# Kernel tuning notes

Hardware: AMD Instinct MI355X
Metric: run time of the kernel (lower is better)

## Reference

```python
import jax, jax.numpy as jnp
import numpy as np

B, T, L, E, H, V = 128, 16, 196, 512, 1024, 32000


def setup_inputs() -> dict:
    key = jax.random.key(0)
    ks = jax.random.split(key, 20)
    s = 0.02
    return {
        "caption_in": jax.random.randint(ks[0], (B, T), 0, V),
        "image_feats": jax.random.normal(ks[1], (B, L, E), jnp.float32),
        "emb": jax.random.normal(ks[2], (V, E), jnp.float32) * s,
        "W_init_h": jax.random.normal(ks[3], (E, H), jnp.float32) * s,
        "b_init_h": jnp.zeros((H,), jnp.float32),
        "W_init_c": jax.random.normal(ks[4], (E, H), jnp.float32) * s,
        "b_init_c": jnp.zeros((H,), jnp.float32),
        "W_a": jax.random.normal(ks[5], (H, H), jnp.float32) * s,
        "b_a": jnp.zeros((H,), jnp.float32),
        "U_a": jax.random.normal(ks[6], (E, H), jnp.float32) * s,
        "b_ua": jnp.zeros((H,), jnp.float32),
        "V_a": jax.random.normal(ks[7], (H, 1), jnp.float32) * s,
        "b_va": jnp.zeros((1,), jnp.float32),
        "W_beta": jax.random.normal(ks[8], (H, E), jnp.float32) * s,
        "b_beta": jnp.zeros((E,), jnp.float32),
        "W_lstm": jax.random.normal(ks[9], (2 * E, 4 * H), jnp.float32) * s,
        "U_lstm": jax.random.normal(ks[10], (H, 4 * H), jnp.float32) * s,
        "b_lstm": jnp.zeros((4 * H,), jnp.float32),
        "W_out": jax.random.normal(ks[11], (H, V), jnp.float32) * s,
        "b_out": jnp.zeros((V,), jnp.float32),
    }


def _decode(caption_in, image_feats, emb, W_init_h, b_init_h, W_init_c, b_init_c,
            W_a, b_a, U_a, b_ua, V_a, b_va, W_beta, b_beta,
            W_lstm, U_lstm, b_lstm, W_out, b_out):
    cap_emb = emb[caption_in]                      # [B,T,E]
    mean_a = jnp.mean(image_feats, axis=1)         # [B,E]
    h0 = mean_a @ W_init_h + b_init_h              # [B,H]
    c0 = mean_a @ W_init_c + b_init_c
    # attention keys: precompute U_a(h_list) once (same math as in-loop)
    keys = jnp.einsum('ble,eh->blh', image_feats, U_a) + b_ua  # [B,L,H]

    def step(carry, x_t):                          # x_t: [B,E]
        h, c = carry
        q = h @ W_a + b_a                          # [B,H]
        e = jax.nn.relu(q[:, None, :] + keys) @ V_a + b_va  # [B,L,1]
        alpha = jax.nn.softmax(e, axis=1)          # [B,L,1]
        z = jnp.sum(alpha * image_feats, axis=1)   # [B,E]
        z = z * jax.nn.sigmoid(h @ W_beta + b_beta)
        ctx = jnp.concatenate([z, x_t], axis=-1)   # [B,2E]
        gates = ctx @ W_lstm + h @ U_lstm + b_lstm # [B,4H]
        i, f, g, o = jnp.split(gates, 4, axis=-1)  # keras order i,f,c,o
        c_new = jax.nn.sigmoid(f) * c + jax.nn.sigmoid(i) * jnp.tanh(g)
        h_new = jax.nn.sigmoid(o) * jnp.tanh(c_new)
        out = jax.nn.softmax(h_new @ W_out + b_out, axis=-1)  # [B,V]
        return (h_new, c_new), out

    xs = jnp.transpose(cap_emb, (1, 0, 2))         # [T,B,E]
    _, outs = jax.lax.scan(step, (h0, c0), xs)     # [T,B,V]
    return jnp.transpose(outs, (1, 0, 2))          # [B,T,V]


def reference(caption_in, image_feats, emb, W_init_h, b_init_h, W_init_c, b_init_c,
              W_a, b_a, U_a, b_ua, V_a, b_va, W_beta, b_beta,
              W_lstm, U_lstm, b_lstm, W_out, b_out):
    return _decode(caption_in, image_feats, emb, W_init_h, b_init_h, W_init_c, b_init_c,
                   W_a, b_a, U_a, b_ua, V_a, b_va, W_beta, b_beta,
                   W_lstm, U_lstm, b_lstm, W_out, b_out)
```

## Files before the change

kernel.cpp:

```cpp
#include <hip/hip_runtime.h>
#include <hip/hip_bf16.h>
#include <math.h>

constexpr int Bc = 128, Tc = 16, Lc = 196, Ec = 512, Hc = 1024, Vc = 32000;

typedef float f32x4_t __attribute__((ext_vector_type(4)));
typedef short s16x8_t __attribute__((ext_vector_type(8)));

__device__ __forceinline__ float sigmoidf_(float x) { return 1.0f / (1.0f + expf(-x)); }

__device__ __forceinline__ unsigned short bf16rn(float x) {
    union { float f; unsigned u; } v; v.f = x;
    unsigned r = v.u + 0x7fffu + ((v.u >> 16) & 1u);
    return (unsigned short)(r >> 16);
}
__device__ __forceinline__ float bf16tof(unsigned short h) {
    union { unsigned u; float f; } v; v.u = ((unsigned)h) << 16; return v.f;
}

__global__ __launch_bounds__(256)
void transpose_split(const float* __restrict__ src, int N,
                     unsigned short* __restrict__ dhi, unsigned short* __restrict__ dlo,
                     int ldd)
{
    __shared__ float tile[32][33];
    const int k0 = blockIdx.x * 32, n0 = blockIdx.y * 32;
    const int tx = threadIdx.x & 31, ty = threadIdx.x >> 5;
#pragma unroll
    for (int i = 0; i < 4; ++i)
        tile[ty + i * 8][tx] = src[(size_t)(k0 + ty + i * 8) * N + n0 + tx];
    __syncthreads();
#pragma unroll
    for (int i = 0; i < 4; ++i) {
        int nl = ty + i * 8;
        float v = tile[tx][nl];
        unsigned short hi = bf16rn(v);
        unsigned short lo = bf16rn(v - bf16tof(hi));
        size_t off = (size_t)(n0 + nl) * ldd + k0 + tx;
        dhi[off] = hi;
        dlo[off] = lo;
    }
}

__global__ __launch_bounds__(256)
void gemm_mfma_split(const float* __restrict__ A, int lda,
                     const unsigned short* __restrict__ Bhi,
                     const unsigned short* __restrict__ Blo,
                     float* __restrict__ C, long ldc,
                     const float* __restrict__ bias, int K, long cslice)
{
    __shared__ __align__(16) unsigned short As_hi[2][128][32];
    __shared__ __align__(16) unsigned short As_lo[2][128][32];
    __shared__ __align__(16) unsigned short Bs_hi[2][128][32];
    __shared__ __align__(16) unsigned short Bs_lo[2][128][32];

    const int t = threadIdx.x;
    const int wave = t >> 6, lane = t & 63;
    const int wr = wave >> 1, wc = wave & 1;
    const int lm = lane & 15, qd = lane >> 4;
    const size_t m0 = (size_t)blockIdx.x * 128;
    const size_t n0 = (size_t)blockIdx.y * 128;

    const int S   = gridDim.z;
    const int ksl = blockIdx.z;
    const int Ksl = K / S;
    const int kbase = ksl * Ksl;

    const int srow = t >> 1;
    const int skh  = (t & 1) * 16;

    const float* Ap = A + (m0 + srow) * (size_t)lda + skh + kbase;
    const unsigned short* Bhp = Bhi + (n0 + srow) * (size_t)K + skh + kbase;
    const unsigned short* Blp = Blo + (n0 + srow) * (size_t)K + skh + kbase;

    const int nk = Ksl >> 5;
    float* Cp = C + (size_t)ksl * cslice;

    f32x4_t acc[4][4];
#pragma unroll
    for (int i = 0; i < 4; ++i)
#pragma unroll
        for (int j = 0; j < 4; ++j)
            acc[i][j] = (f32x4_t){0.f, 0.f, 0.f, 0.f};

    float av[16];
    s16x8_t sbh0, sbh1, sbl0, sbl1;

#define G_LOAD(k0_)                                              \
    do {                                                         \
        *(float4*)&av[0]  = *(const float4*)(Ap + (k0_));        \
        *(float4*)&av[4]  = *(const float4*)(Ap + (k0_) + 4);    \
        *(float4*)&av[8]  = *(const float4*)(Ap + (k0_) + 8);    \
        *(float4*)&av[12] = *(const float4*)(Ap + (k0_) + 12);   \
        sbh0 = *(const s16x8_t*)(Bhp + (k0_));                   \
        sbh1 = *(const s16x8_t*)(Bhp + (k0_) + 8);               \
        sbl0 = *(const s16x8_t*)(Blp + (k0_));                   \
        sbl1 = *(const s16x8_t*)(Blp + (k0_) + 8);               \
    } while (0)

#define LDS_STORE(buf_)                                          \
    do {                                                         \
        s16x8_t h0, h1, l0, l1;                                  \
        _Pragma("unroll")                                        \
        for (int i = 0; i < 8; ++i) {                            \
            unsigned short hi = bf16rn(av[i]);                   \
            h0[i] = (short)hi;                                   \
            l0[i] = (short)bf16rn(av[i] - bf16tof(hi));          \
        }                                                        \
        _Pragma("unroll")                                        \
        for (int i = 0; i < 8; ++i) {                            \
            unsigned short hi = bf16rn(av[8 + i]);               \
            h1[i] = (short)hi;                                   \
            l1[i] = (short)bf16rn(av[8 + i] - bf16tof(hi));      \
        }                                                        \
        *(s16x8_t*)&As_hi[buf_][srow][skh]     = h0;             \
        *(s16x8_t*)&As_hi[buf_][srow][skh + 8] = h1;             \
        *(s16x8_t*)&As_lo[buf_][srow][skh]     = l0;             \
        *(s16x8_t*)&As_lo[buf_][srow][skh + 8] = l1;             \
        *(s16x8_t*)&Bs_hi[buf_][srow][skh]     = sbh0;           \
        *(s16x8_t*)&Bs_hi[buf_][srow][skh + 8] = sbh1;           \
        *(s16x8_t*)&Bs_lo[buf_][srow][skh]     = sbl0;           \
        *(s16x8_t*)&Bs_lo[buf_][srow][skh + 8] = sbl1;           \
    } while (0)

    G_LOAD(0);
    LDS_STORE(0);
    if (nk > 1) G_LOAD(32);
    __syncthreads();

    for (int k = 0; k < nk; ++k) {
        const int cur = k & 1;
        s16x8_t ah[4], al[4], bh[4], bl[4];
#pragma unroll
        for (int mt = 0; mt < 4; ++mt) {
            ah[mt] = *(const s16x8_t*)&As_hi[cur][wr * 64 + mt * 16 + lm][qd * 8];
            al[mt] = *(const s16x8_t*)&As_lo[cur][wr * 64 + mt * 16 + lm][qd * 8];
        }
#pragma unroll
        for (int nt = 0; nt < 4; ++nt) {
            bh[nt] = *(const s16x8_t*)&Bs_hi[cur][wc * 64 + nt * 16 + lm][qd * 8];
            bl[nt] = *(const s16x8_t*)&Bs_lo[cur][wc * 64 + nt * 16 + lm][qd * 8];
        }
        if (k + 1 < nk) {
            LDS_STORE(cur ^ 1);
            if (k + 2 < nk) G_LOAD((k + 2) << 5);
        }
#pragma unroll
        for (int mt = 0; mt < 4; ++mt)
#pragma unroll
            for (int nt = 0; nt < 4; ++nt) {
                acc[mt][nt] = __builtin_amdgcn_mfma_f32_16x16x32_bf16(ah[mt], bh[nt], acc[mt][nt], 0, 0, 0);
                acc[mt][nt] = __builtin_amdgcn_mfma_f32_16x16x32_bf16(ah[mt], bl[nt], acc[mt][nt], 0, 0, 0);
                acc[mt][nt] = __builtin_amdgcn_mfma_f32_16x16x32_bf16(al[mt], bh[nt], acc[mt][nt], 0, 0, 0);
            }
        __syncthreads();
    }
#undef G_LOAD
#undef LDS_STORE

#pragma unroll
    for (int nt = 0; nt < 4; ++nt) {
        size_t n = n0 + wc * 64 + nt * 16 + lm;
        float bs = bias ? bias[n] : 0.f;
#pragma unroll
        for (int mt = 0; mt < 4; ++mt) {
#pragma unroll
            for (int r = 0; r < 4; ++r) {
                size_t m = m0 + wr * 64 + mt * 16 + qd * 4 + r;
                Cp[(size_t)m * ldc + n] = acc[mt][nt][r] + bs;
            }
        }
    }
}

__global__ __launch_bounds__(256)
void concat2(const float* __restrict__ a, int na, const float* __restrict__ b, int nb,
             float* __restrict__ out)
{
    int i = blockIdx.x * 256 + threadIdx.x;
    if (i < na) out[i] = a[i];
    else if (i < na + nb) out[i] = b[i - na];
}

__global__ __launch_bounds__(256)
void mean_kernel(const float* __restrict__ feats, float* __restrict__ mean_a)
{
    int b = blockIdx.x;
    int e = blockIdx.y * 256 + threadIdx.x;
    const float* f = feats + ((size_t)b * Lc) * Ec + e;
    float s = 0.f;
    for (int l = 0; l < Lc; ++l) s += f[(size_t)l * Ec];
    mean_a[b * Ec + e] = s * (1.0f / Lc);
}

__global__ __launch_bounds__(256)
void att_scores_sk(const float* __restrict__ qp, long qstride,
                   const float* __restrict__ b_a,
                   const float* __restrict__ keys,
                   const float* __restrict__ V_a, const float* __restrict__ b_va,
                   float* __restrict__ e)
{
    int pair = blockIdx.x * 4 + (threadIdx.x >> 6);
    int lane = threadIdx.x & 63;
    int b = pair / Lc;
    const float* kp = keys + (size_t)pair * Hc;
    const float* q0 = qp + (size_t)b * 1536;
    float s = 0.f;
    for (int h = lane; h < Hc; h += 64) {
        float q = b_a[h] + q0[h] + q0[qstride + h] + q0[2 * qstride + h] + q0[3 * qstride + h];
        s = fmaf(fmaxf(q + kp[h], 0.f), V_a[h], s);
    }
#pragma unroll
    for (int off = 32; off > 0; off >>= 1) s += __shfl_down(s, off);
    if (lane == 0) e[pair] = s + b_va[0];
}

__global__ __launch_bounds__(256)
void zxcat_fused(const float* __restrict__ e,
                 const float* __restrict__ qp, long qstride,
                 const float* __restrict__ b_beta,
                 const int* __restrict__ caption, const float* __restrict__ emb,
                 const float* __restrict__ feats, const float* __restrict__ hc,
                 float* __restrict__ xcat, int t)
{
    int b = blockIdx.x;
    int j = blockIdx.y * 256 + threadIdx.x;
    if (blockIdx.y < 2) {
        __shared__ float red[256];
        __shared__ float alpha[Lc];
        int tid = threadIdx.x;
        float ev = (tid < Lc) ? e[b * Lc + tid] : -1e30f;
        red[tid] = ev; __syncthreads();
        for (int s = 128; s > 0; s >>= 1) { if (tid < s) red[tid] = fmaxf(red[tid], red[tid + s]); __syncthreads(); }
        float m = red[0]; __syncthreads();
        float ex = (tid < Lc) ? expf(ev - m) : 0.f;
        red[tid] = ex; __syncthreads();
        for (int s = 128; s > 0; s >>= 1) { if (tid < s) red[tid] += red[tid + s]; __syncthreads(); }
        float ssum = red[0];
        if (tid < Lc) alpha[tid] = ex / ssum;
        __syncthreads();
        const float* f = feats + ((size_t)b * Lc) * Ec + j;
        float s = 0.f;
        for (int l = 0; l < Lc; ++l) s = fmaf(alpha[l], f[(size_t)l * Ec], s);
        const float* q0 = qp + (size_t)b * 1536 + 1024 + j;
        float sb = b_beta[j] + q0[0] + q0[qstride] + q0[2 * qstride] + q0[3 * qstride];
        xcat[(size_t)b * 2048 + j] = s * sigmoidf_(sb);
    } else if (j < 2 * Ec) {
        int tok = caption[b * Tc + t];
        xcat[(size_t)b * 2048 + j] = emb[(size_t)tok * Ec + (j - Ec)];
    } else {
        xcat[(size_t)b * 2048 + j] = hc[(size_t)b * 2048 + (j - 2 * Ec)];
    }
}

__global__ __launch_bounds__(256)
void lstm_elem_sk(const float* __restrict__ gp, long gstride,
                  const float* __restrict__ b_lstm,
                  float* __restrict__ hbase, float* __restrict__ cbase, int ld)
{
    int idx = blockIdx.x * 256 + threadIdx.x;
    int b = idx >> 10;
    int j = idx & (Hc - 1);
    float gi = b_lstm[j], gf = b_lstm[Hc + j], gg = b_lstm[2 * Hc + j], go = b_lstm[3 * Hc + j];
#pragma unroll
    for (int s = 0; s < 4; ++s) {
        const float* g = gp + (size_t)s * gstride + (size_t)b * 4 * Hc;
        gi += g[j]; gf += g[Hc + j]; gg += g[2 * Hc + j]; go += g[3 * Hc + j];
    }
    float* cp = cbase + (size_t)b * ld + j;
    float* hp = hbase + (size_t)b * ld + j;
    float cn = sigmoidf_(gf) * (*cp) + sigmoidf_(gi) * tanhf(gg);
    *cp = cn;
    *hp = sigmoidf_(go) * tanhf(cn);
}

__global__ __launch_bounds__(1024)
void softmax_V(float* __restrict__ out, int t)
{
    int b = blockIdx.x;
    float* p = out + ((size_t)b * Tc + t) * (size_t)Vc;
    __shared__ float red[1024];
    int tid = threadIdx.x;
    float m = -1e30f;
    for (int v = tid; v < Vc; v += 1024) m = fmaxf(m, p[v]);
    red[tid] = m; __syncthreads();
    for (int s = 512; s > 0; s >>= 1) { if (tid < s) red[tid] = fmaxf(red[tid], red[tid + s]); __syncthreads(); }
    m = red[0]; __syncthreads();
    float sum = 0.f;
    for (int v = tid; v < Vc; v += 1024) sum += expf(p[v] - m);
    red[tid] = sum; __syncthreads();
    for (int s = 512; s > 0; s >>= 1) { if (tid < s) red[tid] += red[tid + s]; __syncthreads(); }
    float inv = 1.0f / red[0];
    for (int v = tid; v < Vc; v += 1024) p[v] = expf(p[v] - m) * inv;
}

__global__ __launch_bounds__(256)
void att_scores(const float* __restrict__ q, int ldq, const float* __restrict__ keys,
                const float* __restrict__ V_a, const float* __restrict__ b_va,
                float* __restrict__ e)
{
    int pair = blockIdx.x * 4 + (threadIdx.x >> 6);
    int lane = threadIdx.x & 63;
    int b = pair / Lc;
    const float* qp = q + (size_t)b * ldq;
    const float* kp = keys + (size_t)pair * Hc;
    float s = 0.f;
    for (int h = lane; h < Hc; h += 64)
        s = fmaf(fmaxf(qp[h] + kp[h], 0.f), V_a[h], s);
#pragma unroll
    for (int off = 32; off > 0; off >>= 1) s += __shfl_down(s, off);
    if (lane == 0) e[pair] = s + b_va[0];
}

__global__ __launch_bounds__(256)
void softmax_L(float* __restrict__ e)
{
    int b = blockIdx.x;
    float* p = e + b * Lc;
    __shared__ float red[256];
    int tid = threadIdx.x;
    float m = -1e30f;
    if (tid < Lc) m = p[tid];
    red[tid] = m; __syncthreads();
    for (int s = 128; s > 0; s >>= 1) { if (tid < s) red[tid] = fmaxf(red[tid], red[tid + s]); __syncthreads(); }
    m = red[0]; __syncthreads();
    float ex = 0.f;
    if (tid < Lc) ex = expf(p[tid] - m);
    red[tid] = ex; __syncthreads();
    for (int s = 128; s > 0; s >>= 1) { if (tid < s) red[tid] += red[tid + s]; __syncthreads(); }
    if (tid < Lc) p[tid] = ex / red[0];
}

__global__ __launch_bounds__(256)
void z_kernel(const float* __restrict__ alpha, const float* __restrict__ feats,
              float* __restrict__ z)
{
    int b = blockIdx.x;
    int e = blockIdx.y * 256 + threadIdx.x;
    const float* f = feats + ((size_t)b * Lc) * Ec + e;
    const float* a = alpha + b * Lc;
    float s = 0.f;
    for (int l = 0; l < Lc; ++l) s = fmaf(a[l], f[(size_t)l * Ec], s);
    z[b * Ec + e] = s;
}

__global__ __launch_bounds__(256)
void ctx_build(const float* __restrict__ z, const float* __restrict__ sb,
               const int* __restrict__ caption, const float* __restrict__ emb,
               float* __restrict__ ctx, int t)
{
    int b = blockIdx.x;
    int j = blockIdx.y * 256 + threadIdx.x;
    float v;
    if (j < Ec) {
        v = z[b * Ec + j] * sigmoidf_(sb[b * Ec + j]);
    } else {
        int tok = caption[b * Tc + t];
        v = emb[(size_t)tok * Ec + (j - Ec)];
    }
    ctx[b * (2 * Ec) + j] = v;
}

__global__ __launch_bounds__(256)
void lstm_elem(const float* __restrict__ gates, float* __restrict__ hbase,
               float* __restrict__ cbase, int ld)
{
    int idx = blockIdx.x * 256 + threadIdx.x;
    int b = idx >> 10;
    int j = idx & (Hc - 1);
    const float* g = gates + (size_t)b * 4 * Hc;
    float gi = g[j], gf = g[Hc + j], gg = g[2 * Hc + j], go = g[3 * Hc + j];
    float* cp = cbase + (size_t)b * ld + j;
    float* hp = hbase + (size_t)b * ld + j;
    float cn = sigmoidf_(gf) * (*cp) + sigmoidf_(gi) * tanhf(gg);
    *cp = cn;
    *hp = sigmoidf_(go) * tanhf(cn);
}

__global__ __launch_bounds__(256)
void gemm_f32(const float* __restrict__ A, int lda,
              const float* __restrict__ Bm, int ldb,
              float* __restrict__ C, int ldc,
              const float* __restrict__ bias,
              int K, int accumulate)
{
    __shared__ __align__(16) float As[16][68];
    __shared__ __align__(16) float Bs[16][68];
    const int t  = threadIdx.x;
    const int tx = t & 15;
    const int ty = t >> 4;
    const size_t m0 = (size_t)blockIdx.x * 64;
    const size_t n0 = (size_t)blockIdx.y * 64;
    const int arow = t >> 2;
    const int acol = (t & 3) << 2;
    const int brow = t >> 4;
    const int bcol = (t & 15) << 2;
    const float* Aptr = A + (m0 + arow) * (size_t)lda + acol;
    const float* Bptr = Bm + (size_t)brow * ldb + n0 + bcol;
    float acc[4][4] = {};
    for (int k0 = 0; k0 < K; k0 += 16) {
        float4 av = *reinterpret_cast<const float4*>(Aptr + k0);
        float4 bv = *reinterpret_cast<const float4*>(Bptr + (size_t)k0 * ldb);
        As[acol + 0][arow] = av.x;
        As[acol + 1][arow] = av.y;
        As[acol + 2][arow] = av.z;
        As[acol + 3][arow] = av.w;
        *reinterpret_cast<float4*>(&Bs[brow][bcol]) = bv;
        __syncthreads();
#pragma unroll
        for (int k = 0; k < 16; ++k) {
            float4 a4 = *reinterpret_cast<const float4*>(&As[k][ty << 2]);
            float4 b4 = *reinterpret_cast<const float4*>(&Bs[k][tx << 2]);
            float aa[4] = {a4.x, a4.y, a4.z, a4.w};
            float bb[4] = {b4.x, b4.y, b4.z, b4.w};
#pragma unroll
            for (int i = 0; i < 4; ++i)
#pragma unroll
                for (int j = 0; j < 4; ++j)
                    acc[i][j] = fmaf(aa[i], bb[j], acc[i][j]);
        }
        __syncthreads();
    }
    float4 bv4 = {0.f, 0.f, 0.f, 0.f};
    if (bias) bv4 = *reinterpret_cast<const float4*>(&bias[n0 + (tx << 2)]);
#pragma unroll
    for (int i = 0; i < 4; ++i) {
        size_t off = (m0 + (size_t)(ty << 2) + i) * (size_t)ldc + n0 + (tx << 2);
        float4 o;
        o.x = acc[i][0] + bv4.x;
        o.y = acc[i][1] + bv4.y;
        o.z = acc[i][2] + bv4.z;
        o.w = acc[i][3] + bv4.w;
        if (accumulate) {
            float4 prev = *reinterpret_cast<const float4*>(&C[off]);
            o.x += prev.x; o.y += prev.y; o.z += prev.z; o.w += prev.w;
        }
        *reinterpret_cast<float4*>(&C[off]) = o;
    }
}

extern "C" void kernel_launch(void* const* d_in, const int* in_sizes, int n_in,
                              void* d_out, int out_size, void* d_ws, size_t ws_size,
                              hipStream_t stream)
{
    const int*   caption  = (const int*)  d_in[0];
    const float* feats    = (const float*)d_in[1];
    const float* emb      = (const float*)d_in[2];
    const float* W_init_h = (const float*)d_in[3];
    const float* b_init_h = (const float*)d_in[4];
    const float* W_init_c = (const float*)d_in[5];
    const float* b_init_c = (const float*)d_in[6];
    const float* W_a      = (const float*)d_in[7];
    const float* b_a      = (const float*)d_in[8];
    const float* U_a      = (const float*)d_in[9];
    const float* b_ua     = (const float*)d_in[10];
    const float* V_a      = (const float*)d_in[11];
    const float* b_va     = (const float*)d_in[12];
    const float* W_beta   = (const float*)d_in[13];
    const float* b_beta   = (const float*)d_in[14];
    const float* W_lstm   = (const float*)d_in[15];
    const float* U_lstm   = (const float*)d_in[16];
    const float* b_lstm   = (const float*)d_in[17];
    const float* W_out    = (const float*)d_in[18];
    const float* b_out    = (const float*)d_in[19];
    float* out = (float*)d_out;

    dim3 blk(256);

    char* base = (char*)d_ws;
    size_t off = 0;
    auto alloc = [&](size_t bytes) { char* p = base + off; off = (off + bytes + 15) & ~(size_t)15; return p; };

    float* keys      = (float*)alloc((size_t)Bc * Lc * Hc * 4);
    float* hc        = (float*)alloc((size_t)Bc * 2048 * 4);
    float* qsb_part  = (float*)alloc((size_t)4 * Bc * 1536 * 4);
    float* e         = (float*)alloc((size_t)Bc * Lc * 4);
    float* xcat      = (float*)alloc((size_t)Bc * 2048 * 4);
    float* gate_part = (float*)alloc((size_t)4 * Bc * 4 * Hc * 4);
    float* mean_a    = (float*)alloc((size_t)Bc * Ec * 4);
    float* bcat_i    = (float*)alloc(2048 * 4);
    unsigned short* Wout_hi  = (unsigned short*)alloc((size_t)Vc * Hc * 2);
    unsigned short* Wout_lo  = (unsigned short*)alloc((size_t)Vc * Hc * 2);
    unsigned short* Wg_hi    = (unsigned short*)alloc((size_t)4096 * 2048 * 2);
    unsigned short* Wg_lo    = (unsigned short*)alloc((size_t)4096 * 2048 * 2);
    unsigned short* Wqsb_hi  = (unsigned short*)alloc((size_t)1536 * 1024 * 2);
    unsigned short* Wqsb_lo  = (unsigned short*)alloc((size_t)1536 * 1024 * 2);
    unsigned short* Ua_hi    = (unsigned short*)alloc((size_t)1024 * 512 * 2);
    unsigned short* Ua_lo    = (unsigned short*)alloc((size_t)1024 * 512 * 2);
    unsigned short* Wini_hi  = (unsigned short*)alloc((size_t)2048 * 512 * 2);
    unsigned short* Wini_lo  = (unsigned short*)alloc((size_t)2048 * 512 * 2);
    const size_t need_fast = off;

    const long QSTRIDE = (long)Bc * 1536;
    const long GSTRIDE = (long)Bc * 4 * Hc;

    if (ws_size >= need_fast) {
        transpose_split<<<dim3(16, 32), blk, 0, stream>>>(U_a, 1024, Ua_hi, Ua_lo, 512);
        transpose_split<<<dim3(16, 32), blk, 0, stream>>>(W_init_h, 1024, Wini_hi, Wini_lo, 512);
        transpose_split<<<dim3(16, 32), blk, 0, stream>>>(W_init_c, 1024, Wini_hi + (size_t)1024 * 512, Wini_lo + (size_t)1024 * 512, 512);
        transpose_split<<<dim3(32, 32), blk, 0, stream>>>(W_a, 1024, Wqsb_hi, Wqsb_lo, 1024);
        transpose_split<<<dim3(32, 16), blk, 0, stream>>>(W_beta, 512, Wqsb_hi + (size_t)1024 * 1024, Wqsb_lo + (size_t)1024 * 1024, 1024);
        transpose_split<<<dim3(32, 128), blk, 0, stream>>>(W_lstm, 4096, Wg_hi, Wg_lo, 2048);
        transpose_split<<<dim3(32, 128), blk, 0, stream>>>(U_lstm, 4096, Wg_hi + 1024, Wg_lo + 1024, 2048);
        transpose_split<<<dim3(32, 1000), blk, 0, stream>>>(W_out, Vc, Wout_hi, Wout_lo, 1024);
        concat2<<<dim3(8), blk, 0, stream>>>(b_init_h, 1024, b_init_c, 1024, bcat_i);

        mean_kernel<<<dim3(Bc, 2), blk, 0, stream>>>(feats, mean_a);
        gemm_mfma_split<<<dim3(1, 16, 1), blk, 0, stream>>>(mean_a, Ec, Wini_hi, Wini_lo, hc, 2048, bcat_i, 512, 0);
        gemm_mfma_split<<<dim3((Bc * Lc) / 128, 8, 1), blk, 0, stream>>>(feats, Ec, Ua_hi, Ua_lo, keys, Hc, b_ua, 512, 0);

        for (int t = 0; t < Tc; ++t) {
            gemm_mfma_split<<<dim3(1, 12, 4), blk, 0, stream>>>(hc, 2048, Wqsb_hi, Wqsb_lo, qsb_part, 1536, nullptr, 1024, QSTRIDE);
            att_scores_sk<<<dim3((Bc * Lc) / 4), blk, 0, stream>>>(qsb_part, QSTRIDE, b_a, keys, V_a, b_va, e);
            zxcat_fused<<<dim3(Bc, 8), blk, 0, stream>>>(e, qsb_part, QSTRIDE, b_beta, caption, emb, feats, hc, xcat, t);
            gemm_mfma_split<<<dim3(1, 32, 4), blk, 0, stream>>>(xcat, 2048, Wg_hi, Wg_lo, gate_part, 4096, nullptr, 2048, GSTRIDE);
            lstm_elem_sk<<<dim3((Bc * Hc) / 256), blk, 0, stream>>>(gate_part, GSTRIDE, b_lstm, hc, hc + 1024, 2048);
            gemm_mfma_split<<<dim3(1, 250, 1), blk, 0, stream>>>(hc, 2048, Wout_hi, Wout_lo, out + (size_t)t * Vc, (long)Tc * Vc, b_out, 1024, 0);
            softmax_V<<<dim3(Bc), dim3(1024), 0, stream>>>(out, t);
        }
        return;
    }

    float* ws = (float*)d_ws;
    size_t foff = 0;
    float* l_keys  = ws + foff; foff += (size_t)Bc * Lc * Hc;
    float* l_h     = ws + foff; foff += (size_t)Bc * Hc;
    float* l_c     = ws + foff; foff += (size_t)Bc * Hc;
    float* l_q     = ws + foff; foff += (size_t)Bc * Hc;
    float* l_e     = ws + foff; foff += (size_t)Bc * Lc;
    float* l_sb    = ws + foff; foff += (size_t)Bc * Ec;
    float* l_z     = ws + foff; foff += (size_t)Bc * Ec;
    float* l_ctx   = ws + foff; foff += (size_t)Bc * 2 * Ec;
    float* l_gates = ws + foff; foff += (size_t)Bc * 4 * Hc;
    float* l_mean  = ws + foff; foff += (size_t)Bc * Ec;
    if (ws_size < foff * sizeof(float)) return;

    mean_kernel<<<dim3(Bc, 2), blk, 0, stream>>>(feats, l_mean);
    gemm_f32<<<dim3(Bc / 64, Hc / 64), blk, 0, stream>>>(l_mean, Ec, W_init_h, Hc, l_h, Hc, b_init_h, Ec, 0);
    gemm_f32<<<dim3(Bc / 64, Hc / 64), blk, 0, stream>>>(l_mean, Ec, W_init_c, Hc, l_c, Hc, b_init_c, Ec, 0);
    gemm_f32<<<dim3((Bc * Lc) / 64, Hc / 64), blk, 0, stream>>>(feats, Ec, U_a, Hc, l_keys, Hc, b_ua, Ec, 0);
    for (int t = 0; t < Tc; ++t) {
        gemm_f32<<<dim3(Bc / 64, Hc / 64), blk, 0, stream>>>(l_h, Hc, W_a, Hc, l_q, Hc, b_a, Hc, 0);
        att_scores<<<dim3((Bc * Lc) / 4), blk, 0, stream>>>(l_q, Hc, l_keys, V_a, b_va, l_e);
        softmax_L<<<dim3(Bc), blk, 0, stream>>>(l_e);
        z_kernel<<<dim3(Bc, 2), blk, 0, stream>>>(l_e, feats, l_z);
        gemm_f32<<<dim3(Bc / 64, Ec / 64), blk, 0, stream>>>(l_h, Hc, W_beta, Ec, l_sb, Ec, b_beta, Hc, 0);
        ctx_build<<<dim3(Bc, 4), blk, 0, stream>>>(l_z, l_sb, caption, emb, l_ctx, t);
        gemm_f32<<<dim3(Bc / 64, (4 * Hc) / 64), blk, 0, stream>>>(l_ctx, 2 * Ec, W_lstm, 4 * Hc, l_gates, 4 * Hc, b_lstm, 2 * Ec, 0);
        gemm_f32<<<dim3(Bc / 64, (4 * Hc) / 64), blk, 0, stream>>>(l_h, Hc, U_lstm, 4 * Hc, l_gates, 4 * Hc, nullptr, Hc, 1);
        lstm_elem<<<dim3((Bc * Hc) / 256), blk, 0, stream>>>(l_gates, l_h, l_c, Hc);
        gemm_f32<<<dim3(Bc / 64, Vc / 64), blk, 0, stream>>>(l_h, Hc, W_out, Vc, out + (size_t)t * Vc, Tc * Vc, b_out, Hc, 0);
        softmax_V<<<dim3(Bc), dim3(1024), 0, stream>>>(out, t);
    }
}
```

Baseline: 3.286 ms.

## Merge prep transposes and fuse per-step GEMMs and softmax with attention

All weight transpose/split launches and the mean kernel are merged into one multi-descriptor prep kernel. The next step's q/beta GEMM now runs in the same launch as the vocab projection GEMM, and the vocab softmax shares a launch with the next step's attention scoring. This shifts the schedule so independent work for step t+1 overlaps step t, cutting launch count and filling idle CUs. The cost is a software pipeline that is more complex, plus blocks of mixed size inside one launch.

```diff
diff --git a/kernel.cpp b/kernel.cpp
--- a/kernel.cpp
+++ b/kernel.cpp
@@ -18,17 +18,46 @@
     union { unsigned u; float f; } v; v.u = ((unsigned)h) << 16; return v.f;
 }
 
-__global__ __launch_bounds__(256)
-void transpose_split(const float* __restrict__ src, int N,
-                     unsigned short* __restrict__ dhi, unsigned short* __restrict__ dlo,
-                     int ldd)
-{
+struct TDesc {
+    const float* src;
+    unsigned short* dhi;
+    unsigned short* dlo;
+    int N, ldd, gx, base;
+};
+struct PrepP {
+    TDesc d[8];
+    int tblocks;
+    const float* feats;
+    float* mean_a;
+};
+
+__global__ __launch_bounds__(256)
+void prep_multi(PrepP p)
+{
+    const int id = blockIdx.x;
+    if (id >= p.tblocks) {
+        int idm = id - p.tblocks;
+        int b = idm >> 1;
+        int e = (idm & 1) * 256 + threadIdx.x;
+        const float* f = p.feats + ((size_t)b * Lc) * Ec + e;
+        float s = 0.f;
+        for (int l = 0; l < Lc; ++l) s += f[(size_t)l * Ec];
+        p.mean_a[b * Ec + e] = s * (1.0f / Lc);
+        return;
+    }
+    int di = 0;
+#pragma unroll
+    for (int i = 1; i < 8; ++i) if (id >= p.d[i].base) di = i;
+    const TDesc d = p.d[di];
+    const int lid = id - d.base;
+    const int k0 = (lid % d.gx) * 32;
+    const int n0 = (lid / d.gx) * 32;
+
     __shared__ float tile[32][33];
-    const int k0 = blockIdx.x * 32, n0 = blockIdx.y * 32;
     const int tx = threadIdx.x & 31, ty = threadIdx.x >> 5;
 #pragma unroll
     for (int i = 0; i < 4; ++i)
-        tile[ty + i * 8][tx] = src[(size_t)(k0 + ty + i * 8) * N + n0 + tx];
+        tile[ty + i * 8][tx] = d.src[(size_t)(k0 + ty + i * 8) * d.N + n0 + tx];
     __syncthreads();
 #pragma unroll
     for (int i = 0; i < 4; ++i) {
@@ -36,45 +65,48 @@
         float v = tile[tx][nl];
         unsigned short hi = bf16rn(v);
         unsigned short lo = bf16rn(v - bf16tof(hi));
-        size_t off = (size_t)(n0 + nl) * ldd + k0 + tx;
-        dhi[off] = hi;
-        dlo[off] = lo;
-    }
-}
-
-__global__ __launch_bounds__(256)
-void gemm_mfma_split(const float* __restrict__ A, int lda,
-                     const unsigned short* __restrict__ Bhi,
-                     const unsigned short* __restrict__ Blo,
-                     float* __restrict__ C, long ldc,
-                     const float* __restrict__ bias, int K, long cslice)
-{
-    __shared__ __align__(16) unsigned short As_hi[2][128][32];
-    __shared__ __align__(16) unsigned short As_lo[2][128][32];
-    __shared__ __align__(16) unsigned short Bs_hi[2][128][32];
-    __shared__ __align__(16) unsigned short Bs_lo[2][128][32];
+        size_t off = (size_t)(n0 + nl) * d.ldd + k0 + tx;
+        d.dhi[off] = hi;
+        d.dlo[off] = lo;
+    }
+}
+
+struct GemmP {
+    const float* A;
+    const unsigned short* Bhi;
+    const unsigned short* Blo;
+    float* C;
+    const float* bias;
+    long ldc, cslice;
+    int lda, K, gx, gy, S;
+};
+
+__device__ __forceinline__ void gemm_body(char* smem, int bx, int by, int ksl, const GemmP& p)
+{
+    auto As_hi = (unsigned short (*)[128][32])(smem);
+    auto As_lo = (unsigned short (*)[128][32])(smem + 16384);
+    auto Bs_hi = (unsigned short (*)[128][32])(smem + 32768);
+    auto Bs_lo = (unsigned short (*)[128][32])(smem + 49152);
 
     const int t = threadIdx.x;
     const int wave = t >> 6, lane = t & 63;
     const int wr = wave >> 1, wc = wave & 1;
     const int lm = lane & 15, qd = lane >> 4;
-    const size_t m0 = (size_t)blockIdx.x * 128;
-    const size_t n0 = (size_t)blockIdx.y * 128;
-
-    const int S   = gridDim.z;
-    const int ksl = blockIdx.z;
-    const int Ksl = K / S;
+    const size_t m0 = (size_t)bx * 128;
+    const size_t n0 = (size_t)by * 128;
+
+    const int Ksl = p.K / p.S;
     const int kbase = ksl * Ksl;
 
     const int srow = t >> 1;
     const int skh  = (t & 1) * 16;
 
-    const float* Ap = A + (m0 + srow) * (size_t)lda + skh + kbase;
-    const unsigned short* Bhp = Bhi + (n0 + srow) * (size_t)K + skh + kbase;
-    const unsigned short* Blp = Blo + (n0 + srow) * (size_t)K + skh + kbase;
+    const float* Ap = p.A + (m0 + srow) * (size_t)p.lda + skh + kbase;
+    const unsigned short* Bhp = p.Bhi + (n0 + srow) * (size_t)p.K + skh + kbase;
+    const unsigned short* Blp = p.Blo + (n0 + srow) * (size_t)p.K + skh + kbase;
 
     const int nk = Ksl >> 5;
-    float* Cp = C + (size_t)ksl * cslice;
+    float* Cp = p.C + (size_t)ksl * p.cslice;
 
     f32x4_t acc[4][4];
 #pragma unroll
@@ -161,15 +193,38 @@
 #pragma unroll
     for (int nt = 0; nt < 4; ++nt) {
         size_t n = n0 + wc * 64 + nt * 16 + lm;
-        float bs = bias ? bias[n] : 0.f;
+        float bs = p.bias ? p.bias[n] : 0.f;
 #pragma unroll
         for (int mt = 0; mt < 4; ++mt) {
 #pragma unroll
             for (int r = 0; r < 4; ++r) {
                 size_t m = m0 + wr * 64 + mt * 16 + qd * 4 + r;
-                Cp[(size_t)m * ldc + n] = acc[mt][nt][r] + bs;
+                Cp[(size_t)m * p.ldc + n] = acc[mt][nt][r] + bs;
             }
         }
+    }
+}
+
+__global__ __launch_bounds__(256)
+void gemm_one(GemmP p)
+{
+    __shared__ __align__(16) char smem[65536];
+    gemm_body(smem, blockIdx.x, blockIdx.y, blockIdx.z, p);
+}
+
+__global__ __launch_bounds__(256)
+void gemm_dual(GemmP a, GemmP b)
+{
+    __shared__ __align__(16) char smem[65536];
+    int id = blockIdx.x;
+    const int na = a.gx * a.gy * a.S;
+    if (id < na) {
+        int by = id % a.gy; int bx = (id / a.gy) % a.gx; int kz = id / (a.gy * a.gx);
+        gemm_body(smem, bx, by, kz, a);
+    } else {
+        id -= na;
+        int by = id % b.gy; int bx = (id / b.gy) % b.gx; int kz = id / (b.gy * b.gx);
+        gemm_body(smem, bx, by, kz, b);
     }
 }
 
@@ -213,6 +268,47 @@
 #pragma unroll
     for (int off = 32; off > 0; off >>= 1) s += __shfl_down(s, off);
     if (lane == 0) e[pair] = s + b_va[0];
+}
+
+__global__ __launch_bounds__(1024)
+void smv_att(float* __restrict__ out, int t,
+             const float* __restrict__ qp, long qstride,
+             const float* __restrict__ b_a,
+             const float* __restrict__ keys,
+             const float* __restrict__ V_a, const float* __restrict__ b_va,
+             float* __restrict__ e)
+{
+    __shared__ float red[1024];
+    if (blockIdx.x < 128) {
+        int b = blockIdx.x;
+        float* p = out + ((size_t)b * Tc + t) * (size_t)Vc;
+        int tid = threadIdx.x;
+        float m = -1e30f;
+        for (int v = tid; v < Vc; v += 1024) m = fmaxf(m, p[v]);
+        red[tid] = m; __syncthreads();
+        for (int s = 512; s > 0; s >>= 1) { if (tid < s) red[tid] = fmaxf(red[tid], red[tid + s]); __syncthreads(); }
+        m = red[0]; __syncthreads();
+        float sum = 0.f;
+        for (int v = tid; v < Vc; v += 1024) sum += expf(p[v] - m);
+        red[tid] = sum; __syncthreads();
+        for (int s = 512; s > 0; s >>= 1) { if (tid < s) red[tid] += red[tid + s]; __syncthreads(); }
+        float inv = 1.0f / red[0];
+        for (int v = tid; v < Vc; v += 1024) p[v] = expf(p[v] - m) * inv;
+    } else {
+        int wave = threadIdx.x >> 6, lane = threadIdx.x & 63;
+        int pair = (blockIdx.x - 128) * 16 + wave;
+        int b = pair / Lc;
+        const float* kp = keys + (size_t)pair * Hc;
+        const float* q0 = qp + (size_t)b * 1536;
+        float s = 0.f;
+        for (int h = lane; h < Hc; h += 64) {
+            float q = b_a[h] + q0[h] + q0[qstride + h] + q0[2 * qstride + h] + q0[3 * qstride + h];
+            s = fmaf(fmaxf(q + kp[h], 0.f), V_a[h], s);
+        }
+#pragma unroll
+        for (int off = 32; off > 0; off >>= 1) s += __shfl_down(s, off);
+        if (lane == 0) e[pair] = s + b_va[0];
+    }
 }
 
 __global__ __launch_bounds__(256)
@@ -495,28 +591,53 @@
     const long GSTRIDE = (long)Bc * 4 * Hc;
 
     if (ws_size >= need_fast) {
-        transpose_split<<<dim3(16, 32), blk, 0, stream>>>(U_a, 1024, Ua_hi, Ua_lo, 512);
-        transpose_split<<<dim3(16, 32), blk, 0, stream>>>(W_init_h, 1024, Wini_hi, Wini_lo, 512);
-        transpose_split<<<dim3(16, 32), blk, 0, stream>>>(W_init_c, 1024, Wini_hi + (size_t)1024 * 512, Wini_lo + (size_t)1024 * 512, 512);
-        transpose_split<<<dim3(32, 32), blk, 0, stream>>>(W_a, 1024, Wqsb_hi, Wqsb_lo, 1024);
-        transpose_split<<<dim3(32, 16), blk, 0, stream>>>(W_beta, 512, Wqsb_hi + (size_t)1024 * 1024, Wqsb_lo + (size_t)1024 * 1024, 1024);
-        transpose_split<<<dim3(32, 128), blk, 0, stream>>>(W_lstm, 4096, Wg_hi, Wg_lo, 2048);
-        transpose_split<<<dim3(32, 128), blk, 0, stream>>>(U_lstm, 4096, Wg_hi + 1024, Wg_lo + 1024, 2048);
-        transpose_split<<<dim3(32, 1000), blk, 0, stream>>>(W_out, Vc, Wout_hi, Wout_lo, 1024);
+        PrepP pp;
+        int pb = 0;
+        auto addT = [&](const float* src, int N, unsigned short* dhi, unsigned short* dlo,
+                        int ldd, int gx, int gy, int slot) {
+            pp.d[slot] = TDesc{src, dhi, dlo, N, ldd, gx, pb};
+            pb += gx * gy;
+        };
+        addT(W_out,    Vc,   Wout_hi, Wout_lo, 1024, 32, 1000, 0);
+        addT(W_lstm,   4096, Wg_hi,   Wg_lo,   2048, 32, 128, 1);
+        addT(U_lstm,   4096, Wg_hi + 1024, Wg_lo + 1024, 2048, 32, 128, 2);
+        addT(W_a,      1024, Wqsb_hi, Wqsb_lo, 1024, 32, 32, 3);
+        addT(W_beta,   512,  Wqsb_hi + (size_t)1024 * 1024, Wqsb_lo + (size_t)1024 * 1024, 1024, 32, 16, 4);
+        addT(U_a,      1024, Ua_hi,   Ua_lo,   512, 16, 32, 5);
+        addT(W_init_h, 1024, Wini_hi, Wini_lo, 512, 16, 32, 6);
+        addT(W_init_c, 1024, Wini_hi + (size_t)1024 * 512, Wini_lo + (size_t)1024 * 512, 512, 16, 32, 7);
+        pp.tblocks = pb;
+        pp.feats = feats;
+        pp.mean_a = mean_a;
+        prep_multi<<<dim3(pb + 256), blk, 0, stream>>>(pp);
         concat2<<<dim3(8), blk, 0, stream>>>(b_init_h, 1024, b_init_c, 1024, bcat_i);
 
-        mean_kernel<<<dim3(Bc, 2), blk, 0, stream>>>(feats, mean_a);
-        gemm_mfma_split<<<dim3(1, 16, 1), blk, 0, stream>>>(mean_a, Ec, Wini_hi, Wini_lo, hc, 2048, bcat_i, 512, 0);
-        gemm_mfma_split<<<dim3((Bc * Lc) / 128, 8, 1), blk, 0, stream>>>(feats, Ec, Ua_hi, Ua_lo, keys, Hc, b_ua, 512, 0);
+        auto mkg = [](const float* A, int lda, const unsigned short* bh, const unsigned short* bl,
+                      float* C, long ldc, const float* bias, int K, long cslice,
+                      int gx, int gy, int S) {
+            GemmP p; p.A = A; p.lda = lda; p.Bhi = bh; p.Blo = bl; p.C = C; p.ldc = ldc;
+            p.bias = bias; p.K = K; p.cslice = cslice; p.gx = gx; p.gy = gy; p.S = S; return p;
+        };
+        GemmP g_init = mkg(mean_a, Ec, Wini_hi, Wini_lo, hc, 2048, bcat_i, 512, 0, 1, 16, 1);
+        GemmP g_keys = mkg(feats, Ec, Ua_hi, Ua_lo, keys, Hc, b_ua, 512, 0, 196, 8, 1);
+        GemmP g_qsb  = mkg(hc, 2048, Wqsb_hi, Wqsb_lo, qsb_part, 1536, nullptr, 1024, QSTRIDE, 1, 12, 4);
+        GemmP g_gate = mkg(xcat, 2048, Wg_hi, Wg_lo, gate_part, 4096, nullptr, 2048, GSTRIDE, 1, 32, 4);
+
+        gemm_one<<<dim3(1, 16, 1), blk, 0, stream>>>(g_init);
+        gemm_dual<<<dim3(196 * 8 + 48), blk, 0, stream>>>(g_keys, g_qsb);
+        att_scores_sk<<<dim3((Bc * Lc) / 4), blk, 0, stream>>>(qsb_part, QSTRIDE, b_a, keys, V_a, b_va, e);
 
         for (int t = 0; t < Tc; ++t) {
-            gemm_mfma_split<<<dim3(1, 12, 4), blk, 0, stream>>>(hc, 2048, Wqsb_hi, Wqsb_lo, qsb_part, 1536, nullptr, 1024, QSTRIDE);
-            att_scores_sk<<<dim3((Bc * Lc) / 4), blk, 0, stream>>>(qsb_part, QSTRIDE, b_a, keys, V_a, b_va, e);
             zxcat_fused<<<dim3(Bc, 8), blk, 0, stream>>>(e, qsb_part, QSTRIDE, b_beta, caption, emb, feats, hc, xcat, t);
-            gemm_mfma_split<<<dim3(1, 32, 4), blk, 0, stream>>>(xcat, 2048, Wg_hi, Wg_lo, gate_part, 4096, nullptr, 2048, GSTRIDE);
+            gemm_one<<<dim3(1, 32, 4), blk, 0, stream>>>(g_gate);
             lstm_elem_sk<<<dim3((Bc * Hc) / 256), blk, 0, stream>>>(gate_part, GSTRIDE, b_lstm, hc, hc + 1024, 2048);
-            gemm_mfma_split<<<dim3(1, 250, 1), blk, 0, stream>>>(hc, 2048, Wout_hi, Wout_lo, out + (size_t)t * Vc, (long)Tc * Vc, b_out, 1024, 0);
-            softmax_V<<<dim3(Bc), dim3(1024), 0, stream>>>(out, t);
+            GemmP g_wout = mkg(hc, 2048, Wout_hi, Wout_lo, out + (size_t)t * Vc, (long)Tc * Vc, b_out, 1024, 0, 1, 250, 1);
+            if (t < Tc - 1)
+                gemm_dual<<<dim3(250 + 48), blk, 0, stream>>>(g_wout, g_qsb);
+            else
+                gemm_one<<<dim3(1, 250, 1), blk, 0, stream>>>(g_wout);
+            int natt = (t < Tc - 1) ? (Bc * Lc) / 16 : 0;
+            smv_att<<<dim3(128 + natt), dim3(1024), 0, stream>>>(out, t, qsb_part, QSTRIDE, b_a, keys, V_a, b_va, e);
         }
         return;
     }
```

Result: faster. 2.972 ms (-9.5%).
